# Kernel tuning notes

Measured on AMD Instinct MI355X. Metric: run time of the kernel, lower is better.

Reference implementation:

```python
import jax, jax.numpy as jnp
import numpy as np

B, TV, TE = 128, 32, 64
VOCAB, EMB, H, REPR, NET, MAXLEN = 1024, 256, 512, 128, 8, 32


def setup_inputs() -> dict:
    key = jax.random.key(0)
    ks = jax.random.split(key, 26)
    g = lambda i, shape: jax.random.normal(ks[i], shape, dtype=jnp.float32) * 0.05
    return dict(
        input_vertex=jax.random.randint(ks[0], (B, TV), 0, VOCAB),
        input_edge=jax.random.randint(ks[1], (B, TE, 3), 0, NET),
        vertex_emb=g(2, (VOCAB, EMB)),
        v_Wi=g(3, (3 * H, EMB)), v_Wh=g(4, (3 * H, H)), v_bi=g(5, (3 * H,)), v_bh=g(6, (3 * H,)),
        vout_W=g(7, (VOCAB, H)), vout_b=g(8, (VOCAB,)),
        vrep_W=g(9, (REPR, H)), vrep_b=g(10, (REPR,)),
        edge_emb=g(11, (MAXLEN, EMB)),
        e_Wi=g(12, (3 * H, 2 * EMB)), e_Wh=g(13, (3 * H, H)), e_bi=g(14, (3 * H,)), e_bh=g(15, (3 * H,)),
        erep_W=g(16, (REPR, H)), erep_b=g(17, (REPR,)),
        etype_W=g(18, (NET, REPR)), etype_b=g(19, (NET,)),
        src_w=g(20, (REPR,)), src_b=g(21, ()),
        dst_w=g(22, (REPR,)), dst_b=g(23, ()),
    )


def _gru_scan(X, Wi, Wh, bi, bh):
    # X: [T, B, D] -> hidden states [T, B, H]; torch GRUCell gate order r,z,n
    gi = jnp.einsum('tbd,gd->tbg', X, Wi) + bi  # precompute input projections
    h0 = jnp.zeros((X.shape[1], Wh.shape[1]), X.dtype)

    def step(h, gi_t):
        gh = h @ Wh.T + bh
        ir, iz, inn = jnp.split(gi_t, 3, axis=-1)
        hr, hz, hn = jnp.split(gh, 3, axis=-1)
        r = jax.nn.sigmoid(ir + hr)
        z = jax.nn.sigmoid(iz + hz)
        n = jnp.tanh(inn + r * hn)
        h_new = (1.0 - z) * n + z * h
        return h_new, h_new

    _, hs = jax.lax.scan(step, h0, gi)
    return hs


def reference(input_vertex, input_edge, vertex_emb, v_Wi, v_Wh, v_bi, v_bh,
              vout_W, vout_b, vrep_W, vrep_b, edge_emb, e_Wi, e_Wh, e_bi, e_bh,
              erep_W, erep_b, etype_W, etype_b, src_w, src_b, dst_w, dst_b):
    # ---- vertex RNN ----
    Ve = vertex_emb[input_vertex].transpose(1, 0, 2)          # [Tv, B, emb]
    hv = _gru_scan(Ve, v_Wi, v_Wh, v_bi, v_bh)                # [Tv, B, H]
    O_vertex = jnp.einsum('tbh,vh->bvt', hv, vout_W) + vout_b[None, :, None]  # [B, vocab, Tv]
    vrep = jnp.einsum('tbh,rh->tbr', hv, vrep_W) + vrep_b     # [Tv, B, repr]

    # ---- edge RNN ----
    E = jnp.concatenate([edge_emb[input_edge[:, :, 0]],
                         edge_emb[input_edge[:, :, 1]]], axis=2)  # [B, Te, 2*emb]
    he = _gru_scan(E.transpose(1, 0, 2), e_Wi, e_Wh, e_bi, e_bh)  # [Te, B, H]
    e = jnp.einsum('tbh,rh->tbr', he, erep_W) + erep_b            # [Te, B, repr]
    O_edge_type = jnp.einsum('ebr,kr->bke', e, etype_W) + etype_b[None, :, None]  # [B, n_et, Te]

    # ---- edge-vertex additive attention: tanh(e + v) ----
    u = jnp.tanh(e[:, None] + vrep[None])                     # [Te, Tv, B, repr]
    osrc = jnp.einsum('evbr,r->bve', u, src_w) + src_b        # [B, Tv, Te]
    odst = jnp.einsum('evbr,r->bve', u, dst_w) + dst_b        # [B, Tv, Te]
    O_edge = jnp.stack([osrc, odst], axis=2)                  # [B, Tv, 2, Te]

    return O_vertex, O_edge, O_edge_type
```

## Files before the change

kernel.cpp:

```cpp
#include <hip/hip_runtime.h>
#include <hip/hip_bf16.h>


typedef __bf16 bf16_t;
typedef bf16_t bf16x8 __attribute__((ext_vector_type(8)));
typedef bf16_t bf16x4 __attribute__((ext_vector_type(4)));
typedef float  f32x4  __attribute__((ext_vector_type(4)));

#define OFF_GIV  0ull
#define OFF_GIE  6291456ull
#define OFF_HV   18874368ull
#define OFF_HE   20971520ull
#define OFF_VREP 25165824ull
#define OFF_EREP 25690112ull
#define OFF_HBUF 26738688ull
#define FLAG_BYTE_OFF 54001664ull
#define OFF_CVT  27002880ull
#define CVT_VEMB  0ull
#define CVT_EEMB  262144ull
#define CVT_VWI   270336ull
#define CVT_EWI   663552ull
#define CVT_VWH   1449984ull
#define CVT_EWH   2236416ull
#define CVT_VOUT  3022848ull
#define CVT_VREPW 3547136ull
#define CVT_EREPW 3612672ull

#define OUT_OV 0ull
#define OUT_OE 4194304ull
#define OUT_OT 4718592ull

__device__ __forceinline__ float fsigmoid(float x) {
    float e = __builtin_amdgcn_exp2f(-x * 1.4426950408889634f);
    return __builtin_amdgcn_rcpf(1.0f + e);
}
__device__ __forceinline__ float ftanh(float x) {
    x = fminf(x, 15.0f);
    float e = __builtin_amdgcn_exp2f(x * 2.8853900817779268f);
    return (e - 1.0f) * __builtin_amdgcn_rcpf(e + 1.0f);
}

__global__ __launch_bounds__(256) void prep_kernel(
    const float* __restrict__ vemb, const float* __restrict__ eemb,
    const float* __restrict__ vwi,  const float* __restrict__ ewi,
    const float* __restrict__ vwh,  const float* __restrict__ ewh,
    const float* __restrict__ voutw, const float* __restrict__ vrepw,
    const float* __restrict__ erepw, bf16_t* __restrict__ cvt)
{
    int blk = blockIdx.x;
    const float* src; bf16_t* dst; int lb;
    if (blk < 256)       { src = vemb;  dst = cvt + CVT_VEMB;  lb = blk; }
    else if (blk < 264)  { src = eemb;  dst = cvt + CVT_EEMB;  lb = blk - 256; }
    else if (blk < 648)  { src = vwi;   dst = cvt + CVT_VWI;   lb = blk - 264; }
    else if (blk < 1416) { src = ewi;   dst = cvt + CVT_EWI;   lb = blk - 648; }
    else if (blk < 2184) { src = vwh;   dst = cvt + CVT_VWH;   lb = blk - 1416; }
    else if (blk < 2952) { src = ewh;   dst = cvt + CVT_EWH;   lb = blk - 2184; }
    else if (blk < 3464) { src = voutw; dst = cvt + CVT_VOUT;  lb = blk - 2952; }
    else if (blk < 3528) { src = vrepw; dst = cvt + CVT_VREPW; lb = blk - 3464; }
    else                 { src = erepw; dst = cvt + CVT_EREPW; lb = blk - 3528; }
    int idx = lb * 1024 + threadIdx.x * 4;
    float4 v = *(const float4*)(src + idx);
    bf16x4 o;
    o[0] = (bf16_t)v.x; o[1] = (bf16_t)v.y; o[2] = (bf16_t)v.z; o[3] = (bf16_t)v.w;
    *(bf16x4*)(dst + idx) = o;
}

template<int GATHER, int OUTMODE, int K, int TT, typename CT>
__global__ __launch_bounds__(256) void gemm_bt(
    const bf16_t* __restrict__ A, const bf16_t* __restrict__ W,
    const float* __restrict__ bias, CT* __restrict__ C,
    const int* __restrict__ gidx, const bf16_t* __restrict__ emb, int N)
{
    constexpr int K32 = K / 32;
    const int tid = threadIdx.x, lane = tid & 63, wv = tid >> 6;
    const int r16 = lane & 15, quad = lane >> 4, koff = quad * 8;
    const int mbase = blockIdx.x * 256 + wv * 64;
    const int nbase = blockIdx.y * 64;

    const bf16_t* ap0[4];
    const bf16_t* ap1[4];
#pragma unroll
    for (int i = 0; i < 4; ++i) {
        int row = mbase + i * 16 + r16;
        if (GATHER == 0) {
            ap0[i] = A + (size_t)row * K + koff;
            ap1[i] = ap0[i];
        } else if (GATHER == 1) {
            int idx = gidx[row];
            ap0[i] = emb + (size_t)idx * 256 + koff;
            ap1[i] = ap0[i];
        } else {
            int c = row * 3;
            ap0[i] = emb + (size_t)gidx[c] * 256 + koff;
            ap1[i] = emb + (size_t)gidx[c + 1] * 256 + koff;
        }
    }
    const bf16_t* bp[4];
#pragma unroll
    for (int j = 0; j < 4; ++j)
        bp[j] = W + (size_t)(nbase + j * 16 + r16) * K + koff;

    f32x4 acc[4][4];
#pragma unroll
    for (int i = 0; i < 4; ++i)
#pragma unroll
        for (int j = 0; j < 4; ++j) acc[i][j] = (f32x4){0.f, 0.f, 0.f, 0.f};

    for (int kc = 0; kc < K32; ++kc) {
        bf16x8 a[4], b[4];
#pragma unroll
        for (int i = 0; i < 4; ++i) {
            const bf16_t* p;
            if (GATHER == 2) p = (kc < 8) ? (ap0[i] + kc * 32) : (ap1[i] + (kc - 8) * 32);
            else             p = ap0[i] + kc * 32;
            a[i] = *(const bf16x8*)p;
        }
#pragma unroll
        for (int j = 0; j < 4; ++j) b[j] = *(const bf16x8*)(bp[j] + kc * 32);
#pragma unroll
        for (int i = 0; i < 4; ++i)
#pragma unroll
            for (int j = 0; j < 4; ++j)
                acc[i][j] = __builtin_amdgcn_mfma_f32_16x16x32_bf16(a[i], b[j], acc[i][j], 0, 0, 0);
    }

#pragma unroll
    for (int j = 0; j < 4; ++j) {
        int col = nbase + j * 16 + r16;
        float bf = bias[col];
#pragma unroll
        for (int i = 0; i < 4; ++i) {
            int rowq = mbase + i * 16 + quad * 4;
            if (OUTMODE == 1) {
                int b = rowq >> 5, t0 = rowq & 31;
                float4 v4;
                v4.x = acc[i][j][0] + bf; v4.y = acc[i][j][1] + bf;
                v4.z = acc[i][j][2] + bf; v4.w = acc[i][j][3] + bf;
                *(float4*)((float*)C + ((size_t)(b * 1024) + col) * 32 + t0) = v4;
            } else {
#pragma unroll
                for (int q = 0; q < 4; ++q) {
                    int row = rowq + q;
                    C[(size_t)row * N + col] = (CT)(acc[i][j][q] + bf);
                }
            }
        }
    }
}

__global__ __launch_bounds__(512) void gru_scan(
    const bf16_t* __restrict__ giV, const bf16_t* __restrict__ giE,
    const bf16_t* __restrict__ WhV, const bf16_t* __restrict__ WhE,
    const float* __restrict__ bhV, const float* __restrict__ bhE,
    bf16_t* __restrict__ hV, bf16_t* __restrict__ hE,
    bf16_t* __restrict__ hbuf, int* __restrict__ flags)
{
    const int blk  = blockIdx.x;
    const int role = blk >> 5;
    const int lb   = blk & 31;
    const int g    = lb & 7;
    const int s    = lb >> 3;
    const bf16_t* gi = role ? giE : giV;
    const bf16_t* Wh = role ? WhE : WhV;
    const float*  bh = role ? bhE : bhV;
    bf16_t* hout = role ? hE : hV;
    const int T = role ? 64 : 32;
    const int slot = role * 8 + g;
    bf16_t* buf0 = hbuf + (size_t)slot * 2 * 8192;
    int* fl = flags + slot * 4;
    const int bb = g * 16;

    const int tid = threadIdx.x, lane = tid & 63, wv = tid >> 6;
    const int r16 = lane & 15, quad = lane >> 4, koff = quad * 8;
    const int j = s * 128 + wv * 16 + r16;
    const int rs0 = (s + 1) & 3, rs1 = (s + 2) & 3, rs2 = (s + 3) & 3;

    bf16x8 wfrag[3][16];
#pragma unroll
    for (int gate = 0; gate < 3; ++gate) {
        const bf16_t* wrow = Wh + ((size_t)(gate * 512 + j)) * 512 + koff;
#pragma unroll
        for (int kc = 0; kc < 16; ++kc)
            wfrag[gate][kc] = *(const bf16x8*)(wrow + kc * 32);
    }
    const float bhr = bh[j], bhz = bh[512 + j], bhn = bh[1024 + j];
    float hq[4] = {0.f, 0.f, 0.f, 0.f};

    __shared__ __align__(16) bf16_t hbf[2][16][520];
    for (int i = tid; i < 16 * 512; i += 512)
        hbf[0][i >> 9][i & 511] = (bf16_t)0.f;

    const int arow = tid >> 5, au = tid & 31;

    for (int t = 0; t < T; ++t) {
        float gv[3][4];
#pragma unroll
        for (int gg = 0; gg < 3; ++gg)
#pragma unroll
            for (int q = 0; q < 4; ++q)
                gv[gg][q] = (float)gi[((size_t)((bb + quad * 4 + q) * T + t)) * 1536
                                      + gg * 512 + j];

        if (t > 0) {
            while (!__all((int)(__hip_atomic_load(&fl[lane & 3], __ATOMIC_RELAXED,
                                                  __HIP_MEMORY_SCOPE_AGENT) >= t))) { }
            asm volatile("" ::: "memory");
            unsigned long long* src = (unsigned long long*)(buf0 + (size_t)(t & 1) * 8192);
            unsigned long long vv[3];
            vv[0] = __hip_atomic_load(src + arow * 128 + rs0 * 32 + au, __ATOMIC_RELAXED, __HIP_MEMORY_SCOPE_AGENT);
            vv[1] = __hip_atomic_load(src + arow * 128 + rs1 * 32 + au, __ATOMIC_RELAXED, __HIP_MEMORY_SCOPE_AGENT);
            vv[2] = __hip_atomic_load(src + arow * 128 + rs2 * 32 + au, __ATOMIC_RELAXED, __HIP_MEMORY_SCOPE_AGENT);
            *(unsigned long long*)&hbf[t & 1][arow][rs0 * 128 + au * 4] = vv[0];
            *(unsigned long long*)&hbf[t & 1][arow][rs1 * 128 + au * 4] = vv[1];
            *(unsigned long long*)&hbf[t & 1][arow][rs2 * 128 + au * 4] = vv[2];
        }
        __syncthreads();

        const bf16_t (*cur)[520] = hbf[t & 1];
        f32x4 ar = {0.f,0.f,0.f,0.f}, az = {0.f,0.f,0.f,0.f}, an = {0.f,0.f,0.f,0.f};
#pragma unroll
        for (int kc = 0; kc < 16; ++kc) {
            bf16x8 a = *(const bf16x8*)&cur[r16][kc * 32 + koff];
            ar = __builtin_amdgcn_mfma_f32_16x16x32_bf16(a, wfrag[0][kc], ar, 0, 0, 0);
            az = __builtin_amdgcn_mfma_f32_16x16x32_bf16(a, wfrag[1][kc], az, 0, 0, 0);
            an = __builtin_amdgcn_mfma_f32_16x16x32_bf16(a, wfrag[2][kc], an, 0, 0, 0);
        }

        bf16_t hb4[4];
#pragma unroll
        for (int q = 0; q < 4; ++q) {
            float r = fsigmoid(gv[0][q] + ar[q] + bhr);
            float z = fsigmoid(gv[1][q] + az[q] + bhz);
            float n = ftanh(gv[2][q] + r * (an[q] + bhn));
            float hnew = (1.0f - z) * n + z * hq[q];
            hq[q] = hnew;
            hb4[q] = (bf16_t)hnew;
        }

        bf16_t (*nxt)[520] = hbf[(t + 1) & 1];
#pragma unroll
        for (int q = 0; q < 4; ++q) nxt[quad * 4 + q][j] = hb4[q];

        if (t + 1 < T) {
            bf16_t* dstg = buf0 + (size_t)((t + 1) & 1) * 8192;
#pragma unroll
            for (int q = 0; q < 4; ++q)
                __hip_atomic_store((unsigned short*)(dstg + (quad * 4 + q) * 512 + j),
                                   __builtin_bit_cast(unsigned short, hb4[q]),
                                   __ATOMIC_RELAXED, __HIP_MEMORY_SCOPE_AGENT);
            __builtin_amdgcn_s_waitcnt(0);
            __syncthreads();
            if (tid == 0)
                __hip_atomic_store(&fl[s], t + 1,
                                   __ATOMIC_RELAXED, __HIP_MEMORY_SCOPE_AGENT);
        } else {
            __syncthreads();
        }
#pragma unroll
        for (int q = 0; q < 4; ++q)
            hout[((size_t)((bb + quad * 4 + q) * T + t)) * 512 + j] = hb4[q];
    }
}

__global__ __launch_bounds__(256) void etype_kernel(
    const bf16_t* __restrict__ erep, const float* __restrict__ W,
    const float* __restrict__ bias, float* __restrict__ out)
{
    int o = blockIdx.x * 256 + threadIdx.x;
    int te = o & 63, k = (o >> 6) & 7, b = o >> 9;
    float sacc = bias[k];
    const bf16_t* e = erep + ((size_t)(b * 64 + te)) * 128;
    const float* w = W + k * 128;
#pragma unroll 8
    for (int r = 0; r < 128; ++r) sacc += (float)e[r] * w[r];
    out[OUT_OT + o] = sacc;
}

__global__ __launch_bounds__(256) void attn_kernel(
    const bf16_t* __restrict__ erep, const bf16_t* __restrict__ vrep,
    const float* __restrict__ src_w, const float* __restrict__ src_b,
    const float* __restrict__ dst_w, const float* __restrict__ dst_b,
    float* __restrict__ out)
{
    int b = blockIdx.x >> 1, half = blockIdx.x & 1;
    __shared__ float es[32][129], vs[32][129], swf[128], dwf[128];
    int tid = threadIdx.x;
    for (int f = tid; f < 32 * 128; f += 256) {
        int i = f >> 7, r = f & 127;
        es[i][r] = (float)erep[((size_t)(b * 64 + half * 32 + i)) * 128 + r];
        vs[i][r] = (float)vrep[((size_t)(b * 32 + i)) * 128 + r];
    }
    if (tid < 128) { swf[tid] = src_w[tid]; dwf[tid] = dst_w[tid]; }
    __syncthreads();
    float sb = src_b[0], db = dst_b[0];
    for (int p = tid; p < 1024; p += 256) {
        int te = p & 31, tv = p >> 5;
        float sacc = 0.f, dacc = 0.f;
#pragma unroll 4
        for (int r = 0; r < 128; ++r) {
            float u = ftanh(es[te][r] + vs[tv][r]);
            sacc += u * swf[r];
            dacc += u * dwf[r];
        }
        int teg = half * 32 + te;
        size_t base = OUT_OE + ((size_t)(b * 32 + tv) * 2) * 64;
        out[base + teg]      = sacc + sb;
        out[base + 64 + teg] = dacc + db;
    }
}

extern "C" void kernel_launch(void* const* d_in, const int* in_sizes, int n_in,
                              void* d_out, int out_size, void* d_ws, size_t ws_size,
                              hipStream_t stream)
{
    const int*   input_vertex = (const int*)d_in[0];
    const int*   input_edge   = (const int*)d_in[1];
    const float* vertex_emb   = (const float*)d_in[2];
    const float* v_Wi  = (const float*)d_in[3];
    const float* v_Wh  = (const float*)d_in[4];
    const float* v_bi  = (const float*)d_in[5];
    const float* v_bh  = (const float*)d_in[6];
    const float* vout_W = (const float*)d_in[7];
    const float* vout_b = (const float*)d_in[8];
    const float* vrep_W = (const float*)d_in[9];
    const float* vrep_b = (const float*)d_in[10];
    const float* edge_emb = (const float*)d_in[11];
    const float* e_Wi  = (const float*)d_in[12];
    const float* e_Wh  = (const float*)d_in[13];
    const float* e_bi  = (const float*)d_in[14];
    const float* e_bh  = (const float*)d_in[15];
    const float* erep_W = (const float*)d_in[16];
    const float* erep_b = (const float*)d_in[17];
    const float* etype_W = (const float*)d_in[18];
    const float* etype_b = (const float*)d_in[19];
    const float* src_w = (const float*)d_in[20];
    const float* src_b = (const float*)d_in[21];
    const float* dst_w = (const float*)d_in[22];
    const float* dst_b = (const float*)d_in[23];

    bf16_t* ws   = (bf16_t*)d_ws;
    bf16_t* giV  = ws + OFF_GIV;
    bf16_t* giE  = ws + OFF_GIE;
    bf16_t* hV   = ws + OFF_HV;
    bf16_t* hE   = ws + OFF_HE;
    bf16_t* vrep = ws + OFF_VREP;
    bf16_t* erep = ws + OFF_EREP;
    bf16_t* hbuf = ws + OFF_HBUF;
    bf16_t* cvt  = ws + OFF_CVT;
    int*    flags = (int*)((char*)d_ws + FLAG_BYTE_OFF);
    float*  out  = (float*)d_out;

    prep_kernel<<<3592, 256, 0, stream>>>(vertex_emb, edge_emb, v_Wi, e_Wi, v_Wh, e_Wh,
                                          vout_W, vrep_W, erep_W, cvt);

    gemm_bt<1, 0, 256, 32, bf16_t><<<dim3(16, 24), 256, 0, stream>>>(
        nullptr, cvt + CVT_VWI, v_bi, giV, input_vertex, cvt + CVT_VEMB, 1536);
    gemm_bt<2, 0, 512, 64, bf16_t><<<dim3(32, 24), 256, 0, stream>>>(
        nullptr, cvt + CVT_EWI, e_bi, giE, input_edge, cvt + CVT_EEMB, 1536);

    gru_scan<<<64, 512, 0, stream>>>(giV, giE, cvt + CVT_VWH, cvt + CVT_EWH,
                                     v_bh, e_bh, hV, hE, hbuf, flags);

    gemm_bt<0, 1, 512, 32, float><<<dim3(16, 16), 256, 0, stream>>>(
        hV, cvt + CVT_VOUT, vout_b, out, nullptr, nullptr, 1024);
    gemm_bt<0, 0, 512, 32, bf16_t><<<dim3(16, 2), 256, 0, stream>>>(
        hV, cvt + CVT_VREPW, vrep_b, vrep, nullptr, nullptr, 128);
    gemm_bt<0, 0, 512, 64, bf16_t><<<dim3(32, 2), 256, 0, stream>>>(
        hE, cvt + CVT_EREPW, erep_b, erep, nullptr, nullptr, 128);

    etype_kernel<<<256, 256, 0, stream>>>(erep, etype_W, etype_b, out);
    attn_kernel<<<256, 256, 0, stream>>>(erep, vrep, src_w, src_b, dst_w, dst_b, out);
}
```

Baseline: 470.1 us.

## Fuse GRU input-projection GEMMs into scan kernel with per-timestep readiness counters

The two input-projection GEMMs are folded into the recurrent scan launch as extra producer blocks. The gi layout changes to time-major so each producer tile covers whole timesteps, and each tile bumps a per-timestep atomic counter. Scan blocks spin on that counter before consuming step t, so the recurrence can start while later projections are still being computed and two kernel launches go away. The risk is that correctness now depends on the 64 scan blocks and the producers being co-resident, and on relaxed atomics giving proper ordering. Spinning blocks may also compete with producers for compute units.

```diff
diff --git a/kernel.cpp b/kernel.cpp
--- a/kernel.cpp
+++ b/kernel.cpp
@@ -15,6 +15,7 @@
 #define OFF_EREP 25690112ull
 #define OFF_HBUF 26738688ull
 #define FLAG_BYTE_OFF 54001664ull
+#define GICNT_BYTE_OFF 54001920ull
 #define OFF_CVT  27002880ull
 #define CVT_VEMB  0ull
 #define CVT_EEMB  262144ull
@@ -45,9 +46,14 @@
     const float* __restrict__ vwi,  const float* __restrict__ ewi,
     const float* __restrict__ vwh,  const float* __restrict__ ewh,
     const float* __restrict__ voutw, const float* __restrict__ vrepw,
-    const float* __restrict__ erepw, bf16_t* __restrict__ cvt)
+    const float* __restrict__ erepw, bf16_t* __restrict__ cvt,
+    int* __restrict__ gicnt)
 {
     int blk = blockIdx.x;
+    if (blk >= 3592) {
+        if (threadIdx.x < 96) gicnt[threadIdx.x] = 0;
+        return;
+    }
     const float* src; bf16_t* dst; int lb;
     if (blk < 256)       { src = vemb;  dst = cvt + CVT_VEMB;  lb = blk; }
     else if (blk < 264)  { src = eemb;  dst = cvt + CVT_EEMB;  lb = blk - 256; }
@@ -65,32 +71,28 @@
     *(bf16x4*)(dst + idx) = o;
 }
 
-template<int GATHER, int OUTMODE, int K, int TT, typename CT>
-__global__ __launch_bounds__(256) void gemm_bt(
-    const bf16_t* __restrict__ A, const bf16_t* __restrict__ W,
-    const float* __restrict__ bias, CT* __restrict__ C,
-    const int* __restrict__ gidx, const bf16_t* __restrict__ emb, int N)
+template<int GATHER, int K>
+__device__ __forceinline__ void produce_gi(
+    const bf16_t* __restrict__ W, const float* __restrict__ bias,
+    bf16_t* __restrict__ C, const int* __restrict__ gidx,
+    const bf16_t* __restrict__ emb, int* __restrict__ cnt, int bx, int nbase)
 {
     constexpr int K32 = K / 32;
     const int tid = threadIdx.x, lane = tid & 63, wv = tid >> 6;
     const int r16 = lane & 15, quad = lane >> 4, koff = quad * 8;
-    const int mbase = blockIdx.x * 256 + wv * 64;
-    const int nbase = blockIdx.y * 64;
+    const int mbase = bx * 512 + wv * 64;
 
     const bf16_t* ap0[4];
     const bf16_t* ap1[4];
 #pragma unroll
     for (int i = 0; i < 4; ++i) {
         int row = mbase + i * 16 + r16;
-        if (GATHER == 0) {
-            ap0[i] = A + (size_t)row * K + koff;
-            ap1[i] = ap0[i];
-        } else if (GATHER == 1) {
-            int idx = gidx[row];
-            ap0[i] = emb + (size_t)idx * 256 + koff;
+        int b = row & 127, t = row >> 7;
+        if (GATHER == 1) {
+            ap0[i] = emb + (size_t)gidx[b * 32 + t] * 256 + koff;
             ap1[i] = ap0[i];
         } else {
-            int c = row * 3;
+            int c = (b * 64 + t) * 3;
             ap0[i] = emb + (size_t)gidx[c] * 256 + koff;
             ap1[i] = emb + (size_t)gidx[c + 1] * 256 + koff;
         }
@@ -130,34 +132,50 @@
         float bf = bias[col];
 #pragma unroll
         for (int i = 0; i < 4; ++i) {
-            int rowq = mbase + i * 16 + quad * 4;
-            if (OUTMODE == 1) {
-                int b = rowq >> 5, t0 = rowq & 31;
-                float4 v4;
-                v4.x = acc[i][j][0] + bf; v4.y = acc[i][j][1] + bf;
-                v4.z = acc[i][j][2] + bf; v4.w = acc[i][j][3] + bf;
-                *(float4*)((float*)C + ((size_t)(b * 1024) + col) * 32 + t0) = v4;
-            } else {
-#pragma unroll
-                for (int q = 0; q < 4; ++q) {
-                    int row = rowq + q;
-                    C[(size_t)row * N + col] = (CT)(acc[i][j][q] + bf);
-                }
+#pragma unroll
+            for (int q = 0; q < 4; ++q) {
+                int row = mbase + i * 16 + quad * 4 + q;
+                bf16_t hb = (bf16_t)(acc[i][j][q] + bf);
+                __hip_atomic_store((unsigned short*)(C + (size_t)row * 1536 + col),
+                                   __builtin_bit_cast(unsigned short, hb),
+                                   __ATOMIC_RELAXED, __HIP_MEMORY_SCOPE_AGENT);
             }
         }
     }
-}
-
-__global__ __launch_bounds__(512) void gru_scan(
-    const bf16_t* __restrict__ giV, const bf16_t* __restrict__ giE,
+    __builtin_amdgcn_s_waitcnt(0);
+    __syncthreads();
+    if (tid < 4)
+        __hip_atomic_fetch_add(&cnt[bx * 4 + tid], 1,
+                               __ATOMIC_RELAXED, __HIP_MEMORY_SCOPE_AGENT);
+}
+
+__global__ __launch_bounds__(512) void fused_scan(
+    bf16_t* __restrict__ giV, bf16_t* __restrict__ giE,
     const bf16_t* __restrict__ WhV, const bf16_t* __restrict__ WhE,
     const float* __restrict__ bhV, const float* __restrict__ bhE,
     bf16_t* __restrict__ hV, bf16_t* __restrict__ hE,
-    bf16_t* __restrict__ hbuf, int* __restrict__ flags)
-{
-    const int blk  = blockIdx.x;
-    const int role = blk >> 5;
-    const int lb   = blk & 31;
+    bf16_t* __restrict__ hbuf, int* __restrict__ flags, int* __restrict__ gicnt,
+    const int* __restrict__ ivtx, const int* __restrict__ iedg,
+    const bf16_t* __restrict__ vemb, const bf16_t* __restrict__ eemb,
+    const bf16_t* __restrict__ vwi, const bf16_t* __restrict__ ewi,
+    const float* __restrict__ vbi, const float* __restrict__ ebi)
+{
+    __shared__ __align__(16) bf16_t hbf[2][16][520];
+    const int bid = blockIdx.x;
+
+    if (bid >= 64) {
+        if (bid < 256) {
+            int g2 = bid - 64;
+            produce_gi<1, 256>(vwi, vbi, giV, ivtx, vemb, gicnt, g2 & 7, (g2 >> 3) * 64);
+        } else {
+            int g3 = bid - 256;
+            produce_gi<2, 512>(ewi, ebi, giE, iedg, eemb, gicnt + 32, g3 & 15, (g3 >> 4) * 64);
+        }
+        return;
+    }
+
+    const int role = bid >> 5;
+    const int lb   = bid & 31;
     const int g    = lb & 7;
     const int s    = lb >> 3;
     const bf16_t* gi = role ? giE : giV;
@@ -168,6 +186,7 @@
     const int slot = role * 8 + g;
     bf16_t* buf0 = hbuf + (size_t)slot * 2 * 8192;
     int* fl = flags + slot * 4;
+    int* gc = role ? (gicnt + 32) : gicnt;
     const int bb = g * 16;
 
     const int tid = threadIdx.x, lane = tid & 63, wv = tid >> 6;
@@ -186,19 +205,21 @@
     const float bhr = bh[j], bhz = bh[512 + j], bhn = bh[1024 + j];
     float hq[4] = {0.f, 0.f, 0.f, 0.f};
 
-    __shared__ __align__(16) bf16_t hbf[2][16][520];
     for (int i = tid; i < 16 * 512; i += 512)
         hbf[0][i >> 9][i & 511] = (bf16_t)0.f;
 
     const int arow = tid >> 5, au = tid & 31;
 
     for (int t = 0; t < T; ++t) {
+        while (__hip_atomic_load(&gc[t], __ATOMIC_RELAXED,
+                                 __HIP_MEMORY_SCOPE_AGENT) < 24) { }
+        asm volatile("" ::: "memory");
         float gv[3][4];
 #pragma unroll
         for (int gg = 0; gg < 3; ++gg)
 #pragma unroll
             for (int q = 0; q < 4; ++q)
-                gv[gg][q] = (float)gi[((size_t)((bb + quad * 4 + q) * T + t)) * 1536
+                gv[gg][q] = (float)gi[((size_t)(t * 128 + bb + quad * 4 + q)) * 1536
                                       + gg * 512 + j];
 
         if (t > 0) {
@@ -259,6 +280,67 @@
 #pragma unroll
         for (int q = 0; q < 4; ++q)
             hout[((size_t)((bb + quad * 4 + q) * T + t)) * 512 + j] = hb4[q];
+    }
+}
+
+template<int OUTMODE, int K, int TT, typename CT>
+__global__ __launch_bounds__(256) void gemm_bt(
+    const bf16_t* __restrict__ A, const bf16_t* __restrict__ W,
+    const float* __restrict__ bias, CT* __restrict__ C, int N)
+{
+    constexpr int K32 = K / 32;
+    const int tid = threadIdx.x, lane = tid & 63, wv = tid >> 6;
+    const int r16 = lane & 15, quad = lane >> 4, koff = quad * 8;
+    const int mbase = blockIdx.x * 256 + wv * 64;
+    const int nbase = blockIdx.y * 64;
+
+    const bf16_t* ap0[4];
+#pragma unroll
+    for (int i = 0; i < 4; ++i)
+        ap0[i] = A + (size_t)(mbase + i * 16 + r16) * K + koff;
+    const bf16_t* bp[4];
+#pragma unroll
+    for (int j = 0; j < 4; ++j)
+        bp[j] = W + (size_t)(nbase + j * 16 + r16) * K + koff;
+
+    f32x4 acc[4][4];
+#pragma unroll
+    for (int i = 0; i < 4; ++i)
+#pragma unroll
+        for (int j = 0; j < 4; ++j) acc[i][j] = (f32x4){0.f, 0.f, 0.f, 0.f};
+
+    for (int kc = 0; kc < K32; ++kc) {
+        bf16x8 a[4], b[4];
+#pragma unroll
+        for (int i = 0; i < 4; ++i) a[i] = *(const bf16x8*)(ap0[i] + kc * 32);
+#pragma unroll
+        for (int j = 0; j < 4; ++j) b[j] = *(const bf16x8*)(bp[j] + kc * 32);
+#pragma unroll
+        for (int i = 0; i < 4; ++i)
+#pragma unroll
+            for (int j = 0; j < 4; ++j)
+                acc[i][j] = __builtin_amdgcn_mfma_f32_16x16x32_bf16(a[i], b[j], acc[i][j], 0, 0, 0);
+    }
+
+#pragma unroll
+    for (int j = 0; j < 4; ++j) {
+        int col = nbase + j * 16 + r16;
+        float bf = bias[col];
+#pragma unroll
+        for (int i = 0; i < 4; ++i) {
+            int rowq = mbase + i * 16 + quad * 4;
+            if (OUTMODE == 1) {
+                int b = rowq >> 5, t0 = rowq & 31;
+                float4 v4;
+                v4.x = acc[i][j][0] + bf; v4.y = acc[i][j][1] + bf;
+                v4.z = acc[i][j][2] + bf; v4.w = acc[i][j][3] + bf;
+                *(float4*)((float*)C + ((size_t)(b * 1024) + col) * 32 + t0) = v4;
+            } else {
+#pragma unroll
+                for (int q = 0; q < 4; ++q)
+                    C[(size_t)(rowq + q) * N + col] = (CT)(acc[i][j][q] + bf);
+            }
+        }
     }
 }
 
@@ -348,25 +430,24 @@
     bf16_t* hbuf = ws + OFF_HBUF;
     bf16_t* cvt  = ws + OFF_CVT;
     int*    flags = (int*)((char*)d_ws + FLAG_BYTE_OFF);
+    int*    gicnt = (int*)((char*)d_ws + GICNT_BYTE_OFF);
     float*  out  = (float*)d_out;
 
-    prep_kernel<<<3592, 256, 0, stream>>>(vertex_emb, edge_emb, v_Wi, e_Wi, v_Wh, e_Wh,
-                                          vout_W, vrep_W, erep_W, cvt);
-
-    gemm_bt<1, 0, 256, 32, bf16_t><<<dim3(16, 24), 256, 0, stream>>>(
-        nullptr, cvt + CVT_VWI, v_bi, giV, input_vertex, cvt + CVT_VEMB, 1536);
-    gemm_bt<2, 0, 512, 64, bf16_t><<<dim3(32, 24), 256, 0, stream>>>(
-        nullptr, cvt + CVT_EWI, e_bi, giE, input_edge, cvt + CVT_EEMB, 1536);
-
-    gru_scan<<<64, 512, 0, stream>>>(giV, giE, cvt + CVT_VWH, cvt + CVT_EWH,
-                                     v_bh, e_bh, hV, hE, hbuf, flags);
-
-    gemm_bt<0, 1, 512, 32, float><<<dim3(16, 16), 256, 0, stream>>>(
-        hV, cvt + CVT_VOUT, vout_b, out, nullptr, nullptr, 1024);
-    gemm_bt<0, 0, 512, 32, bf16_t><<<dim3(16, 2), 256, 0, stream>>>(
-        hV, cvt + CVT_VREPW, vrep_b, vrep, nullptr, nullptr, 128);
-    gemm_bt<0, 0, 512, 64, bf16_t><<<dim3(32, 2), 256, 0, stream>>>(
-        hE, cvt + CVT_EREPW, erep_b, erep, nullptr, nullptr, 128);
+    prep_kernel<<<3593, 256, 0, stream>>>(vertex_emb, edge_emb, v_Wi, e_Wi, v_Wh, e_Wh,
+                                          vout_W, vrep_W, erep_W, cvt, gicnt);
+
+    fused_scan<<<640, 512, 0, stream>>>(
+        giV, giE, cvt + CVT_VWH, cvt + CVT_EWH, v_bh, e_bh, hV, hE,
+        hbuf, flags, gicnt, input_vertex, input_edge,
+        cvt + CVT_VEMB, cvt + CVT_EEMB, cvt + CVT_VWI, cvt + CVT_EWI,
+        v_bi, e_bi);
+
+    gemm_bt<1, 512, 32, float><<<dim3(16, 16), 256, 0, stream>>>(
+        hV, cvt + CVT_VOUT, vout_b, out, 1024);
+    gemm_bt<0, 512, 32, bf16_t><<<dim3(16, 2), 256, 0, stream>>>(
+        hV, cvt + CVT_VREPW, vrep_b, vrep, 128);
+    gemm_bt<0, 512, 64, bf16_t><<<dim3(32, 2), 256, 0, stream>>>(
+        hE, cvt + CVT_EREPW, erep_b, erep, 128);
 
     etype_kernel<<<256, 256, 0, stream>>>(erep, etype_W, etype_b, out);
     attn_kernel<<<256, 256, 0, stream>>>(erep, vrep, src_w, src_b, dst_w, dst_b, out);
```

After: 479.7 us. +2.1%, slower.
